# Performance work log

Measured on AMD Instinct MI355X. Metric: run time of the kernel, lower is better.

The kernel has to match this reference:

```python
import jax, jax.numpy as jnp
import numpy as np

N, E1, E2, P, H = 4096, 131072, 131072, 65536, 128
ROLE_VOCAB, ROLE_DIM, IDX_VOCAB, IDX_DIM = 8, 16, 1024, 8


def _lin_init(key, fan_in, fan_out):
    k1, k2 = jax.random.split(key)
    bound = 1.0 / np.sqrt(fan_in)
    W = jax.random.uniform(k1, (fan_in, fan_out), jnp.float32, -bound, bound)
    b = jax.random.uniform(k2, (fan_out,), jnp.float32, -bound, bound)
    return W, b


def setup_inputs() -> dict:
    key = jax.random.key(0)
    ks = jax.random.split(key, 24)
    d = {}
    d["block_features"] = jax.random.normal(ks[0], (N, 16), jnp.float32)
    d["role_ids"] = jax.random.randint(ks[1], (N,), 0, ROLE_VOCAB)
    d["b2b_src"] = jax.random.randint(ks[2], (E1,), 0, N)
    d["b2b_dst"] = jax.random.randint(ks[3], (E1,), 0, N)
    d["b2b_w"] = jax.random.uniform(ks[4], (E1,), jnp.float32)
    d["p2b_pin"] = jax.random.randint(ks[5], (E2,), 0, P)
    d["p2b_block"] = jax.random.randint(ks[6], (E2,), 0, N)
    d["p2b_w"] = jax.random.uniform(ks[7], (E2,), jnp.float32)
    d["pins_pos"] = jax.random.normal(ks[8], (P, 2), jnp.float32)
    d["area_targets"] = jax.random.uniform(ks[9], (N,), jnp.float32)
    # parameters
    d["role_emb"] = jax.random.normal(ks[10], (ROLE_VOCAB, ROLE_DIM), jnp.float32)
    d["idx_emb"] = jax.random.normal(ks[11], (IDX_VOCAB, IDX_DIM), jnp.float32)
    d["in_W1"], d["in_b1"] = _lin_init(ks[12], 16 + IDX_DIM + ROLE_DIM, H)
    d["in_W2"], d["in_b2"] = _lin_init(ks[13], H, H)
    d["b2b_W1"], d["b2b_b1"] = _lin_init(ks[14], 2 * H + 1, H)
    d["b2b_W2"], d["b2b_b2"] = _lin_init(ks[15], H, H)
    d["p2b_W1"], d["p2b_b1"] = _lin_init(ks[16], H + 3, H)
    d["p2b_W2"], d["p2b_b2"] = _lin_init(ks[17], H, H)
    d["self_W"], d["self_b"] = _lin_init(ks[18], H, H)
    d["ln_g"] = jnp.ones((H,), jnp.float32)
    d["ln_b"] = jnp.zeros((H,), jnp.float32)
    d["gp_W1"], d["gp_b1"] = _lin_init(ks[19], 2 * H, H)
    d["gp_W2"], d["gp_b2"] = _lin_init(ks[20], H, H)
    return d


def _mlp2(x, W1, b1, W2, b2):
    return jax.nn.relu(x @ W1 + b1) @ W2 + b2


def _forward(block_features, role_ids, b2b_src, b2b_dst, b2b_w, p2b_pin, p2b_block,
             p2b_w, pins_pos, area_targets, role_emb, idx_emb, in_W1, in_b1, in_W2,
             in_b2, b2b_W1, b2b_b1, b2b_W2, b2b_b2, p2b_W1, p2b_b1, p2b_W2, p2b_b2,
             self_W, self_b, ln_g, ln_b, gp_W1, gp_b1, gp_W2, gp_b2):
    n = block_features.shape[0]
    role_e = role_emb[role_ids]                       # [N, role_dim]
    idx_e = idx_emb[jnp.arange(n) % IDX_VOCAB]        # [N, idx_dim]
    x = jnp.concatenate([block_features, role_e, idx_e], axis=-1)
    h = jax.nn.relu(_mlp2(x, in_W1, in_b1, in_W2, in_b2))  # input_proj ends in ReLU

    # --- b2b messages: two directed messages per undirected edge ---
    max_b2b = jax.lax.stop_gradient(jnp.maximum(jnp.max(jnp.abs(b2b_w)), 1.0))
    w = (b2b_w / max_b2b)[:, None]                    # [E1, 1]
    hi, hj = h[b2b_src], h[b2b_dst]                   # [E1, H]
    m_ij = _mlp2(jnp.concatenate([hi, hj, w], -1), b2b_W1, b2b_b1, b2b_W2, b2b_b2)
    m_ji = _mlp2(jnp.concatenate([hj, hi, w], -1), b2b_W1, b2b_b1, b2b_W2, b2b_b2)
    agg = jnp.zeros_like(h).at[b2b_src].add(m_ij).at[b2b_dst].add(m_ji)

    # --- p2b messages ---
    total_area = jnp.maximum(jnp.sum(area_targets), 1e-6)
    case_scale = jax.lax.stop_gradient(jnp.maximum(jnp.sqrt(total_area), 1e-6))
    max_p2b = jax.lax.stop_gradient(jnp.maximum(jnp.max(jnp.abs(p2b_w)), 1.0))
    pin_feats = jnp.concatenate(
        [pins_pos[p2b_pin] / case_scale, (p2b_w / max_p2b)[:, None]], axis=-1)  # [E2, 3]
    m_p = _mlp2(jnp.concatenate([h[p2b_block], pin_feats], -1),
                p2b_W1, p2b_b1, p2b_W2, p2b_b2)
    agg = agg.at[p2b_block].add(m_p)

    # --- combine + LayerNorm ---
    z = h @ self_W + self_b + agg
    mu = jnp.mean(z, axis=-1, keepdims=True)
    var = jnp.mean(jnp.square(z - mu), axis=-1, keepdims=True)
    block_embeddings = (z - mu) / jnp.sqrt(var + 1e-5) * ln_g + ln_b

    pooled = jnp.concatenate(
        [block_embeddings.mean(axis=0), block_embeddings.max(axis=0)], axis=-1)
    graph_embedding = _mlp2(pooled, gp_W1, gp_b1, gp_W2, gp_b2)
    return block_embeddings, graph_embedding


def reference(block_features, role_ids, b2b_src, b2b_dst, b2b_w, p2b_pin, p2b_block,
              p2b_w, pins_pos, area_targets, role_emb, idx_emb, in_W1, in_b1, in_W2,
              in_b2, b2b_W1, b2b_b1, b2b_W2, b2b_b2, p2b_W1, p2b_b1, p2b_W2, p2b_b2,
              self_W, self_b, ln_g, ln_b, gp_W1, gp_b1, gp_W2, gp_b2):
    block_embeddings, graph_embedding = _forward(
        block_features, role_ids, b2b_src, b2b_dst, b2b_w, p2b_pin, p2b_block,
        p2b_w, pins_pos, area_targets, role_emb, idx_emb, in_W1, in_b1, in_W2,
        in_b2, b2b_W1, b2b_b1, b2b_W2, b2b_b2, p2b_W1, p2b_b1, p2b_W2, p2b_b2,
        self_W, self_b, ln_g, ln_b, gp_W1, gp_b1, gp_W2, gp_b2)
    block_mask = jnp.ones((block_features.shape[0],), dtype=bool)
    return block_embeddings, graph_embedding, block_mask
```

## Files before the change

kernel.cpp:

```cpp
#include <hip/hip_runtime.h>
#include <hip/hip_bf16.h>

#define N_NODES 4096
#define HDIM    128
#define E1      131072
#define E2      131072
#define NMSG_B2B (2 * E1)
#define CAPB    192
#define CAPP    96
#define STGB    128
#define STGP    64

#define OFF_CNTB   8
#define OFF_CNTP   (OFF_CNTB + 4096)
#define OFF_RED    (OFF_CNTP + 4096)
#define OFF_PSUM   (OFF_RED + 96)
#define OFF_PMAX   (OFF_PSUM + 512)
#define OFF_HB     (OFF_PMAX + 512)
#define OFF_P      (OFF_HB + 262144)
#define OFF_Q      (OFF_P + 524288)
#define OFF_R      (OFF_Q + 524288)
#define OFF_CP     (OFF_R + 524288)
#define OFF_B2H    (OFF_CP + 24576)
#define OFF_B2L    (OFF_B2H + 8192)
#define OFF_P2H    (OFF_B2L + 8192)
#define OFF_P2L    (OFF_P2H + 8192)
#define OFF_SWP    (OFF_P2L + 8192)
#define OFF_IW1    (OFF_SWP + 8192)
#define OFF_IW2    (OFF_IW1 + 4096)
#define OFF_WLAST  (OFF_IW2 + 8192)
#define OFF_PEXTRA (OFF_WLAST + 128)
#define OFF_BKB    (OFF_PEXTRA + 384)
#define OFF_BKP    (OFF_BKB + 2 * N_NODES * CAPB)
#define WS_FLOATS  (OFF_BKP + 2 * N_NODES * CAPP)

typedef short short8 __attribute__((ext_vector_type(8)));
typedef float f32x4 __attribute__((ext_vector_type(4)));

__device__ __forceinline__ unsigned short f2bf(float f) {
  union { float f; unsigned u; } v; v.f = f;
  unsigned r = v.u + 0x7fffu + ((v.u >> 16) & 1u);
  return (unsigned short)(r >> 16);
}
__device__ __forceinline__ float bf2f(unsigned short h) {
  return __uint_as_float((unsigned)h << 16);
}
__device__ __forceinline__ int il(int c) { return ((c & 63) << 1) | (c >> 6); }
__device__ __forceinline__ f32x4 relu4(f32x4 v) {
  f32x4 r;
  r[0] = fmaxf(v[0], 0.f); r[1] = fmaxf(v[1], 0.f);
  r[2] = fmaxf(v[2], 0.f); r[3] = fmaxf(v[3], 0.f);
  return r;
}

__global__ __launch_bounds__(256) void setup_kernel(const float* __restrict__ b2bw,
                                                    const float* __restrict__ p2bw,
                                                    const float* __restrict__ area,
                                                    const float* __restrict__ bW1,
                                                    const float* __restrict__ bW2,
                                                    const float* __restrict__ pW1,
                                                    const float* __restrict__ pW2,
                                                    const float* __restrict__ sWm,
                                                    const float* __restrict__ iW1,
                                                    const float* __restrict__ iW2,
                                                    const int* __restrict__ src,
                                                    const int* __restrict__ dst,
                                                    const int* __restrict__ pblk,
                                                    const int* __restrict__ ppin,
                                                    const float* __restrict__ pins,
                                                    float* __restrict__ ws) {
  __shared__ float red[256];
  int b = blockIdx.x, t = threadIdx.x;
  if (b < 32) {
    float m = 0.f;
    for (int i = b * 256 + t; i < E1; i += 32 * 256) m = fmaxf(m, fabsf(b2bw[i]));
    red[t] = m; __syncthreads();
    for (int s = 128; s > 0; s >>= 1) { if (t < s) red[t] = fmaxf(red[t], red[t + s]); __syncthreads(); }
    if (t == 0) ws[OFF_RED + b] = red[0];
  } else if (b < 64) {
    float m = 0.f;
    for (int i = (b - 32) * 256 + t; i < E2; i += 32 * 256) m = fmaxf(m, fabsf(p2bw[i]));
    red[t] = m; __syncthreads();
    for (int s = 128; s > 0; s >>= 1) { if (t < s) red[t] = fmaxf(red[t], red[t + s]); __syncthreads(); }
    if (t == 0) ws[OFF_RED + b] = red[0];
  } else if (b < 96) {
    float s0 = 0.f;
    for (int i = (b - 64) * 256 + t; i < N_NODES; i += 32 * 256) s0 += area[i];
    red[t] = s0; __syncthreads();
    for (int s = 128; s > 0; s >>= 1) { if (t < s) red[t] += red[t + s]; __syncthreads(); }
    if (t == 0) ws[OFF_RED + b] = red[0];
  } else if (b == 96) {
    for (int i = t; i < 512; i += 256) {
      ws[OFF_PSUM + i] = 0.f;
      ((int*)ws)[OFF_PMAX + i] = 0x80000000;
    }
  } else if (b < 225) {
    unsigned short* Cp  = (unsigned short*)(ws + OFF_CP);
    unsigned short* B2h = (unsigned short*)(ws + OFF_B2H);
    unsigned short* B2l = (unsigned short*)(ws + OFF_B2L);
    unsigned short* P2h = (unsigned short*)(ws + OFF_P2H);
    unsigned short* P2l = (unsigned short*)(ws + OFF_P2L);
    unsigned short* Swp = (unsigned short*)(ws + OFF_SWP);
    unsigned short* I1p = (unsigned short*)(ws + OFF_IW1);
    unsigned short* I2p = (unsigned short*)(ws + OFF_IW2);
    float* wlast = ws + OFF_WLAST;
    float* pextra = ws + OFF_PEXTRA;
    const int total = 156160;
    for (int x = (b - 97) * 256 + t; x < total; x += 128 * 256) {
      if (x < 49152) {
        int j = x & 7, lane = (x >> 3) & 63, ks = (x >> 9) & 3, nc = x >> 11;
        int col = nc * 16 + (lane & 15), k = ks * 32 + (lane >> 4) * 8 + j;
        float v;
        if (col < 128)      v = bW1[k * 128 + col];
        else if (col < 256) v = bW1[(128 + k) * 128 + (col - 128)];
        else                v = pW1[k * 128 + (col - 256)];
        Cp[x] = f2bf(v);
      } else if (x < 114688) {
        int u = (x - 49152) & 16383, which = (x - 49152) >> 14;
        int j = u & 7, lane = (u >> 3) & 63, ks = (u >> 9) & 3, nt = u >> 11;
        int n = nt * 16 + (lane & 15), k = ks * 32 + (lane >> 4) * 8 + j;
        float v = (which < 2) ? bW2[k * 128 + n] : pW2[k * 128 + n];
        unsigned short hi = f2bf(v);
        unsigned short outv = (which & 1) ? f2bf(v - bf2f(hi)) : hi;
        ((which < 2) ? ((which & 1) ? B2l : B2h) : ((which & 1) ? P2l : P2h))[u] = outv;
      } else if (x < 131072) {
        int u = x - 114688;
        int j = u & 7, lane = (u >> 3) & 63, ks = (u >> 9) & 3, nt = u >> 11;
        int n = nt * 16 + (lane & 15), k = ks * 32 + (lane >> 4) * 8 + j;
        Swp[u] = f2bf(sWm[k * 128 + n]);
      } else if (x < 139264) {
        int u = x - 131072;
        int j = u & 7, lane = (u >> 3) & 63, ks = (u >> 9) & 1, nt = u >> 10;
        int n = nt * 16 + (lane & 15), k = ks * 32 + (lane >> 4) * 8 + j;
        I1p[u] = (k < 40) ? f2bf(iW1[k * 128 + n]) : 0;
      } else if (x < 155648) {
        int u = x - 139264;
        int j = u & 7, lane = (u >> 3) & 63, ks = (u >> 9) & 3, nt = u >> 11;
        int n = nt * 16 + (lane & 15), k = ks * 32 + (lane >> 4) * 8 + j;
        I2p[u] = f2bf(iW2[k * 128 + n]);
      } else if (x < 155776) {
        int c = x - 155648;
        wlast[il(c)] = bW1[256 * 128 + c];
      } else {
        int u = x - 155776;
        int r = u >> 7, c = u & 127;
        pextra[r * 128 + il(c)] = pW1[(128 + r) * 128 + c];
      }
    }
  } else {
    int i = (b - 225) * 256 + t;
    int* cntB = (int*)ws + OFF_CNTB;
    int* cntP = (int*)ws + OFF_CNTP;
    uint2* BKB = (uint2*)((int*)ws + OFF_BKB);
    uint2* BKP = (uint2*)((int*)ws + OFF_BKP);
    if (i < NMSG_B2B) {
      int e = i >> 1, d = i & 1;
      int tg = d ? dst[e] : src[e];
      int o  = d ? src[e] : dst[e];
      int pos = atomicAdd(&cntB[tg], 1);
      if (pos < CAPB) {
        uint2 v; v.x = (unsigned)o; v.y = __float_as_uint(b2bw[e]);
        BKB[tg * CAPB + pos] = v;
      }
    } else {
      int e = i - NMSG_B2B;
      int pin = ppin[e];
      int tg = pblk[e];
      int pos = atomicAdd(&cntP[tg], 1);
      if (pos < CAPP) {
        uint2 v;
        v.x = ((unsigned)f2bf(pins[pin * 2 + 1]) << 16) | (unsigned)f2bf(pins[pin * 2]);
        v.y = __float_as_uint(p2bw[e]);
        BKP[tg * CAPP + pos] = v;
      }
    }
  }
}

__global__ __launch_bounds__(512) void mid_kernel(const float* __restrict__ bfeat,
                                                  const int* __restrict__ rid,
                                                  const float* __restrict__ remb,
                                                  const float* __restrict__ iemb,
                                                  const float* __restrict__ ib1,
                                                  const float* __restrict__ ib2,
                                                  const float* __restrict__ bb1,
                                                  const float* __restrict__ pb1,
                                                  float* __restrict__ ws,
                                                  unsigned short* __restrict__ hb) {
  __shared__ __attribute__((aligned(16))) unsigned short xs[16 * 72];
  __shared__ __attribute__((aligned(16))) unsigned short h1s[16 * 136];
  __shared__ __attribute__((aligned(16))) unsigned short hs[16 * 136];
  int tid = threadIdx.x;
  const unsigned short* I1p = (const unsigned short*)(ws + OFF_IW1);
  const unsigned short* I2p = (const unsigned short*)(ws + OFF_IW2);
  const unsigned short* Cp  = (const unsigned short*)(ws + OFF_CP);
  float* P = ws + OFF_P;
  float* Q = ws + OFF_Q;
  float* R = ws + OFF_R;
  int n0 = blockIdx.x * 16;
  for (int idx = tid; idx < 1024; idx += 512) {
    int m = idx >> 6, c = idx & 63;
    int n = n0 + m;
    float v = 0.f;
    if (c < 16)      v = bfeat[n * 16 + c];
    else if (c < 32) v = remb[rid[n] * 16 + (c - 16)];
    else if (c < 40) v = iemb[(n & 1023) * 8 + (c - 32)];
    xs[m * 72 + c] = f2bf(v);
  }
  __syncthreads();
  int lane = tid & 63, wv = tid >> 6;
  int l15 = lane & 15, q = lane >> 4;
  f32x4 zero = {0.f, 0.f, 0.f, 0.f};
  f32x4 a1 = zero;
#pragma unroll
  for (int ks = 0; ks < 2; ks++) {
    short8 af = *(const short8*)(&xs[l15 * 72 + ks * 32 + q * 8]);
    short8 bfr = *(const short8*)(I1p + ((wv * 2 + ks) * 64 + lane) * 8);
    a1 = __builtin_amdgcn_mfma_f32_16x16x32_bf16(af, bfr, a1, 0, 0, 0);
  }
  {
    int n = wv * 16 + l15;
    float b = ib1[n];
#pragma unroll
    for (int r = 0; r < 4; r++)
      h1s[(q * 4 + r) * 136 + n] = f2bf(fmaxf(a1[r] + b, 0.f));
  }
  __syncthreads();
  f32x4 a2 = zero;
#pragma unroll
  for (int ks = 0; ks < 4; ks++) {
    short8 af = *(const short8*)(&h1s[l15 * 136 + ks * 32 + q * 8]);
    short8 bfr = *(const short8*)(I2p + ((wv * 4 + ks) * 64 + lane) * 8);
    a2 = __builtin_amdgcn_mfma_f32_16x16x32_bf16(af, bfr, a2, 0, 0, 0);
  }
  {
    int n = wv * 16 + l15;
    float b = ib2[n];
#pragma unroll
    for (int r = 0; r < 4; r++) {
      unsigned short hv = f2bf(fmaxf(a2[r] + b, 0.f));
      hs[(q * 4 + r) * 136 + n] = hv;
      hb[(n0 + q * 4 + r) * 128 + n] = hv;
    }
  }
  __syncthreads();
  f32x4 a3[3];
#pragma unroll
  for (int i = 0; i < 3; i++) a3[i] = zero;
#pragma unroll
  for (int ks = 0; ks < 4; ks++) {
    short8 af = *(const short8*)(&hs[l15 * 136 + ks * 32 + q * 8]);
#pragma unroll
    for (int j = 0; j < 3; j++) {
      short8 bfr = *(const short8*)(Cp + (((3 * wv + j) * 4 + ks) * 64 + lane) * 8);
      a3[j] = __builtin_amdgcn_mfma_f32_16x16x32_bf16(af, bfr, a3[j], 0, 0, 0);
    }
  }
#pragma unroll
  for (int j = 0; j < 3; j++) {
    int col = (3 * wv + j) * 16 + l15;
    int arr = col >> 7, cc = col & 127;
    float bias = (arr == 0) ? bb1[cc] : ((arr == 2) ? pb1[cc] : 0.f);
    float* dstp = (arr == 0) ? P : ((arr == 1) ? Q : R);
    int ic = il(cc);
#pragma unroll
    for (int r = 0; r < 4; r++)
      dstp[(n0 + q * 4 + r) * 128 + ic] = a3[j][r] + bias;
  }
}

__global__ __launch_bounds__(1024) void fused_kernel(const unsigned short* __restrict__ hb,
                                                     const float* __restrict__ sb,
                                                     const float* __restrict__ lng,
                                                     const float* __restrict__ lnb,
                                                     const float* __restrict__ bb2,
                                                     const float* __restrict__ pb2,
                                                     const float* __restrict__ gW1,
                                                     const float* __restrict__ gb1,
                                                     const float* __restrict__ gW2,
                                                     const float* __restrict__ gb2,
                                                     float* __restrict__ ws,
                                                     float* __restrict__ out) {
  __shared__ __attribute__((aligned(16))) unsigned short A[16 * 648];
  __shared__ __attribute__((aligned(16))) union {
    struct { float zp[2][16 * 128]; float zs[16 * 133]; } t;
    struct { uint2 bkb[16][STGB]; uint2 bkp[16][STGP]; } e;
  } U;
  __shared__ float muS[16], rsg[16];
  __shared__ float partS[16][16], partQ[16][16];
  __shared__ float psumL[8][128];
  __shared__ int   pmaxL[8][128];
  __shared__ float sInvB, sInvP, sInvC;
  __shared__ int   isLast;
  int tid = threadIdx.x;
  int n0 = blockIdx.x * 16;
  int lane = tid & 63, wv = tid >> 6;
  const int* cntBp = (const int*)ws + OFF_CNTB;
  const int* cntPp = (const int*)ws + OFF_CNTP;
  const uint2* BKB = (const uint2*)((const int*)ws + OFF_BKB);
  const uint2* BKP = (const uint2*)((const int*)ws + OFF_BKP);
  if (tid < 256) {
    int m = tid >> 4, o = (tid & 15) * 8;
    *(uint4*)(&A[m * 648 + o]) = *(const uint4*)(hb + (n0 + m) * 128 + o);
  }
  for (int idx = tid; idx < 16 * STGB; idx += 1024) {
    int m = idx >> 7, j = idx & (STGB - 1);
    if (j < cntBp[n0 + m]) U.e.bkb[m][j] = BKB[(n0 + m) * CAPB + j];
  }
  {
    int m = tid >> 6, j = tid & (STGP - 1);
    if (tid < 16 * STGP && j < cntPp[n0 + m]) U.e.bkp[m][j] = BKP[(n0 + m) * CAPP + j];
  }
  if (tid < 96) {
    float v = ws[OFF_RED + tid];
    if (tid < 64) {
#pragma unroll
      for (int s = 1; s < 32; s <<= 1) v = fmaxf(v, __shfl_xor(v, s, 64));
      if (tid == 0)  sInvB = 1.f / fmaxf(v, 1.f);
      if (tid == 32) sInvP = 1.f / fmaxf(v, 1.f);
    } else {
#pragma unroll
      for (int s = 1; s < 32; s <<= 1) v += __shfl_xor(v, s, 64);
      if (tid == 64) {
        float cs = fmaxf(sqrtf(fmaxf(v, 1e-6f)), 1e-6f);
        sInvC = 1.f / cs;
      }
    }
  }
  int l5 = lane & 31, hf = lane >> 5;
  f32x4 wl = *(const f32x4*)(ws + OFF_WLAST + 4 * l5);
  f32x4 e0 = *(const f32x4*)(ws + OFF_PEXTRA + 4 * l5);
  f32x4 e1 = *(const f32x4*)(ws + OFF_PEXTRA + 128 + 4 * l5);
  f32x4 e2 = *(const f32x4*)(ws + OFF_PEXTRA + 256 + 4 * l5);
  __syncthreads();
  {
    const float* Pm = ws + OFF_P;
    const float* Qm = ws + OFF_Q;
    const float* Rm = ws + OFF_R;
    float invb = sInvB, invp = sInvP, invc = sInvC;
    wl *= invb; e0 *= invc; e1 *= invc; e2 *= invp;
    int ln = wv;
    int node = n0 + ln;
    {
      int cnt = min(cntBp[node], CAPB);
      int stg = min(cnt, STGB);
      const uint2* bkL = U.e.bkb[ln];
      const uint2* bkG = BKB + node * CAPB;
      f32x4 p4 = *(const f32x4*)(Pm + node * 128 + 4 * l5);
      f32x4 acc = {0.f, 0.f, 0.f, 0.f};
      int m = 0;
      for (; m + 16 <= stg; m += 16) {
        uint2 k0 = bkL[m + hf],      k1 = bkL[m + 2 + hf];
        uint2 k2 = bkL[m + 4 + hf],  k3 = bkL[m + 6 + hf];
        uint2 k4 = bkL[m + 8 + hf],  k5 = bkL[m + 10 + hf];
        uint2 k6 = bkL[m + 12 + hf], k7 = bkL[m + 14 + hf];
        f32x4 q0 = *(const f32x4*)(Qm + k0.x * 128 + 4 * l5);
        f32x4 q1 = *(const f32x4*)(Qm + k1.x * 128 + 4 * l5);
        f32x4 q2 = *(const f32x4*)(Qm + k2.x * 128 + 4 * l5);
        f32x4 q3 = *(const f32x4*)(Qm + k3.x * 128 + 4 * l5);
        f32x4 q4 = *(const f32x4*)(Qm + k4.x * 128 + 4 * l5);
        f32x4 q5 = *(const f32x4*)(Qm + k5.x * 128 + 4 * l5);
        f32x4 q6 = *(const f32x4*)(Qm + k6.x * 128 + 4 * l5);
        f32x4 q7 = *(const f32x4*)(Qm + k7.x * 128 + 4 * l5);
        acc += relu4(p4 + __uint_as_float(k0.y) * wl + q0);
        acc += relu4(p4 + __uint_as_float(k1.y) * wl + q1);
        acc += relu4(p4 + __uint_as_float(k2.y) * wl + q2);
        acc += relu4(p4 + __uint_as_float(k3.y) * wl + q3);
        acc += relu4(p4 + __uint_as_float(k4.y) * wl + q4);
        acc += relu4(p4 + __uint_as_float(k5.y) * wl + q5);
        acc += relu4(p4 + __uint_as_float(k6.y) * wl + q6);
        acc += relu4(p4 + __uint_as_float(k7.y) * wl + q7);
      }
      for (; m + 8 <= stg; m += 8) {
        uint2 k0 = bkL[m + hf],     k1 = bkL[m + 2 + hf];
        uint2 k2 = bkL[m + 4 + hf], k3 = bkL[m + 6 + hf];
        f32x4 q0 = *(const f32x4*)(Qm + k0.x * 128 + 4 * l5);
        f32x4 q1 = *(const f32x4*)(Qm + k1.x * 128 + 4 * l5);
        f32x4 q2 = *(const f32x4*)(Qm + k2.x * 128 + 4 * l5);
        f32x4 q3 = *(const f32x4*)(Qm + k3.x * 128 + 4 * l5);
        acc += relu4(p4 + __uint_as_float(k0.y) * wl + q0);
        acc += relu4(p4 + __uint_as_float(k1.y) * wl + q1);
        acc += relu4(p4 + __uint_as_float(k2.y) * wl + q2);
        acc += relu4(p4 + __uint_as_float(k3.y) * wl + q3);
      }
      for (; m + 2 <= stg; m += 2) {
        uint2 k = bkL[m + hf];
        f32x4 q = *(const f32x4*)(Qm + k.x * 128 + 4 * l5);
        acc += relu4(p4 + __uint_as_float(k.y) * wl + q);
      }
      if (m < stg) {
        uint2 k = bkL[m + hf];
        f32x4 q = *(const f32x4*)(Qm + (k.x & (N_NODES - 1)) * 128 + 4 * l5);
        f32x4 v = relu4(p4 + __uint_as_float(k.y) * wl + q);
        if (hf == 0) acc += v;
        m++;
      }
      for (; m + 2 <= cnt; m += 2) {
        uint2 k = bkG[m + hf];
        f32x4 q = *(const f32x4*)(Qm + k.x * 128 + 4 * l5);
        acc += relu4(p4 + __uint_as_float(k.y) * wl + q);
      }
      if (m < cnt) {
        uint2 k = bkG[m + hf];
        f32x4 q = *(const f32x4*)(Qm + (k.x & (N_NODES - 1)) * 128 + 4 * l5);
        f32x4 v = relu4(p4 + __uint_as_float(k.y) * wl + q);
        if (hf == 0) acc += v;
      }
      f32x4 tot;
#pragma unroll
      for (int j = 0; j < 4; j++) tot[j] = acc[j] + __shfl_xor(acc[j], 32, 64);
      if (hf == 0) {
        unsigned short h0 = f2bf(tot[0]), h1 = f2bf(tot[1]);
        unsigned short h2 = f2bf(tot[2]), h3 = f2bf(tot[3]);
        *(unsigned*)(&A[ln * 648 + 128 + 2 * l5])      = (unsigned)h0 | ((unsigned)h2 << 16);
        *(unsigned*)(&A[ln * 648 + 128 + 64 + 2 * l5]) = (unsigned)h1 | ((unsigned)h3 << 16);
        unsigned short g0 = f2bf(tot[0] - bf2f(h0)), g1 = f2bf(tot[1] - bf2f(h1));
        unsigned short g2 = f2bf(tot[2] - bf2f(h2)), g3 = f2bf(tot[3] - bf2f(h3));
        *(unsigned*)(&A[ln * 648 + 256 + 2 * l5])      = (unsigned)g0 | ((unsigned)g2 << 16);
        *(unsigned*)(&A[ln * 648 + 256 + 64 + 2 * l5]) = (unsigned)g1 | ((unsigned)g3 << 16);
      }
    }
    {
      int cnt = min(cntPp[node], CAPP);
      int stg = min(cnt, STGP);
      const uint2* bkL = U.e.bkp[ln];
      const uint2* bkG = BKP + node * CAPP;
      f32x4 r4 = *(const f32x4*)(Rm + node * 128 + 4 * l5);
      f32x4 acc = {0.f, 0.f, 0.f, 0.f};
      int m = 0;
      for (; m + 4 <= stg; m += 4) {
        uint2 ka = bkL[m + hf], kb = bkL[m + 2 + hf];
        float a0 = __uint_as_float((ka.x & 0xFFFFu) << 16);
        float a1 = __uint_as_float(ka.x & 0xFFFF0000u);
        float a2 = __uint_as_float(ka.y);
        float b0 = __uint_as_float((kb.x & 0xFFFFu) << 16);
        float b1 = __uint_as_float(kb.x & 0xFFFF0000u);
        float b2 = __uint_as_float(kb.y);
        acc += relu4(r4 + a0 * e0 + a1 * e1 + a2 * e2);
        acc += relu4(r4 + b0 * e0 + b1 * e1 + b2 * e2);
      }
      for (; m + 2 <= stg; m += 2) {
        uint2 ka = bkL[m + hf];
        float a0 = __uint_as_float((ka.x & 0xFFFFu) << 16);
        float a1 = __uint_as_float(ka.x & 0xFFFF0000u);
        float a2 = __uint_as_float(ka.y);
        acc += relu4(r4 + a0 * e0 + a1 * e1 + a2 * e2);
      }
      if (m < stg) {
        uint2 ka = bkL[m + hf];
        float a0 = __uint_as_float((ka.x & 0xFFFFu) << 16);
        float a1 = __uint_as_float(ka.x & 0xFFFF0000u);
        float a2 = __uint_as_float(ka.y);
        f32x4 v = relu4(r4 + a0 * e0 + a1 * e1 + a2 * e2);
        if (hf == 0) acc += v;
        m++;
      }
      for (; m + 2 <= cnt; m += 2) {
        uint2 ka = bkG[m + hf];
        float a0 = __uint_as_float((ka.x & 0xFFFFu) << 16);
        float a1 = __uint_as_float(ka.x & 0xFFFF0000u);
        float a2 = __uint_as_float(ka.y);
        acc += relu4(r4 + a0 * e0 + a1 * e1 + a2 * e2);
      }
      if (m < cnt) {
        uint2 ka = bkG[m + hf];
        float a0 = __uint_as_float((ka.x & 0xFFFFu) << 16);
        float a1 = __uint_as_float(ka.x & 0xFFFF0000u);
        float a2 = __uint_as_float(ka.y);
        f32x4 v = relu4(r4 + a0 * e0 + a1 * e1 + a2 * e2);
        if (hf == 0) acc += v;
      }
      f32x4 tot;
#pragma unroll
      for (int j = 0; j < 4; j++) tot[j] = acc[j] + __shfl_xor(acc[j], 32, 64);
      if (hf == 0) {
        unsigned short h0 = f2bf(tot[0]), h1 = f2bf(tot[1]);
        unsigned short h2 = f2bf(tot[2]), h3 = f2bf(tot[3]);
        *(unsigned*)(&A[ln * 648 + 384 + 2 * l5])      = (unsigned)h0 | ((unsigned)h2 << 16);
        *(unsigned*)(&A[ln * 648 + 384 + 64 + 2 * l5]) = (unsigned)h1 | ((unsigned)h3 << 16);
        unsigned short g0 = f2bf(tot[0] - bf2f(h0)), g1 = f2bf(tot[1] - bf2f(h1));
        unsigned short g2 = f2bf(tot[2] - bf2f(h2)), g3 = f2bf(tot[3] - bf2f(h3));
        *(unsigned*)(&A[ln * 648 + 512 + 2 * l5])      = (unsigned)g0 | ((unsigned)g2 << 16);
        *(unsigned*)(&A[ln * 648 + 512 + 64 + 2 * l5]) = (unsigned)g1 | ((unsigned)g3 << 16);
      }
    }
  }
  __syncthreads();
  int l15 = lane & 15, q = lane >> 4;
  int ct = wv & 7, half = wv >> 3;
  f32x4 zero = {0.f, 0.f, 0.f, 0.f};
  f32x4 acc = zero;
  const unsigned short* bufs[7] = {
    (const unsigned short*)(ws + OFF_SWP), (const unsigned short*)(ws + OFF_B2H),
    (const unsigned short*)(ws + OFF_B2L), (const unsigned short*)(ws + OFF_B2H),
    (const unsigned short*)(ws + OFF_P2H), (const unsigned short*)(ws + OFF_P2L),
    (const unsigned short*)(ws + OFF_P2H)};
  const int segs[7] = {0, 128, 128, 256, 384, 384, 512};
  int p0 = half ? 4 : 0, p1 = half ? 7 : 4;
  for (int p = p0; p < p1; p++) {
#pragma unroll
    for (int ks = 0; ks < 4; ks++) {
      short8 af = *(const short8*)(&A[l15 * 648 + segs[p] + ks * 32 + q * 8]);
      short8 bfr = *(const short8*)(bufs[p] + ((ct * 4 + ks) * 64 + lane) * 8);
      acc = __builtin_amdgcn_mfma_f32_16x16x32_bf16(af, bfr, acc, 0, 0, 0);
    }
  }
  {
    int nn = ct * 16 + l15;
#pragma unroll
    for (int r = 0; r < 4; r++)
      U.t.zp[half][(q * 4 + r) * 128 + nn] = acc[r];
  }
  __syncthreads();
  {
    int idx = tid;
    for (int rep = 0; rep < 2; rep++, idx += 1024) {
      int row = idx >> 7, c = idx & 127;
      float cb = (float)cntBp[n0 + row], cp = (float)cntPp[n0 + row];
      U.t.zs[row * 133 + c] = U.t.zp[0][row * 128 + c] + U.t.zp[1][row * 128 + c]
                            + sb[c] + cb * bb2[c] + cp * pb2[c];
    }
  }
  __syncthreads();
  if (tid < 256) {
    int r = tid >> 4, g = tid & 15;
    const float* zr = &U.t.zs[r * 133 + g * 8];
    float s = 0.f, s2 = 0.f;
#pragma unroll
    for (int i = 0; i < 8; i++) { float v = zr[i]; s += v; s2 += v * v; }
    partS[r][g] = s; partQ[r][g] = s2;
  }
  __syncthreads();
  if (tid < 16) {
    float s = 0.f, s2 = 0.f;
#pragma unroll
    for (int g = 0; g < 16; g++) { s += partS[tid][g]; s2 += partQ[tid][g]; }
    float m = s * (1.f / 128.f);
    float var = s2 * (1.f / 128.f) - m * m;
    muS[tid] = m;
    rsg[tid] = rsqrtf(fmaxf(var, 0.f) + 1e-5f);
  }
  __syncthreads();
  {
    int c = tid & 127, grp = tid >> 7;
    float g = lng[c], b = lnb[c];
    float ls = 0.f; int lm = 0x80000000;
    for (int r = grp * 2; r < grp * 2 + 2; r++) {
      float v = (U.t.zs[r * 133 + c] - muS[r]) * rsg[r] * g + b;
      out[(n0 + r) * 128 + c] = v;
      ls += v;
      int e = __float_as_int(v);
      e = e >= 0 ? e : (e ^ 0x7fffffff);
      lm = max(lm, e);
    }
    psumL[grp][c] = ls; pmaxL[grp][c] = lm;
  }
  __syncthreads();
  if (tid < 128) {
    float s = 0.f; int mx = 0x80000000;
#pragma unroll
    for (int g = 0; g < 8; g++) { s += psumL[g][tid]; mx = max(mx, pmaxL[g][tid]); }
    int bank = (blockIdx.x & 3) << 7;
    atomicAdd(&ws[OFF_PSUM + bank + tid], s);
    atomicMax(&((int*)ws)[OFF_PMAX + bank + tid], mx);
  }
  if (tid < 16) out[N_NODES * HDIM + HDIM + n0 + tid] = 1.0f;
  __syncthreads();
  if (tid == 0) {
    __threadfence();
    int v = atomicAdd(&((int*)ws)[3], 1);
    isLast = (v == (int)gridDim.x - 1);
  }
  __syncthreads();
  if (!isLast) return;
  __shared__ float pooled[256];
  __shared__ float gpart[8][128];
  __shared__ float g1[128];
  if (tid < 128) {
    float s = 0.f;
#pragma unroll
    for (int bk = 0; bk < 4; bk++) s += atomicAdd(&ws[OFF_PSUM + bk * 128 + tid], 0.f);
    pooled[tid] = s * (1.f / (float)N_NODES);
  } else if (tid < 256) {
    int c = tid - 128;
    int mx = 0x80000000;
#pragma unroll
    for (int bk = 0; bk < 4; bk++) mx = max(mx, atomicAdd(&((int*)ws)[OFF_PMAX + bk * 128 + c], 0));
    int bits = mx >= 0 ? mx : (mx ^ 0x7fffffff);
    pooled[tid] = __int_as_float(bits);
  }
  __syncthreads();
  {
    int c = tid & 127, g = tid >> 7;
    float acc2 = 0.f;
#pragma unroll 8
    for (int k = g * 32; k < g * 32 + 32; k++) acc2 += pooled[k] * gW1[k * 128 + c];
    gpart[g][c] = acc2;
  }
  __syncthreads();
  if (tid < 128) {
    float s = gb1[tid];
#pragma unroll
    for (int g = 0; g < 8; g++) s += gpart[g][tid];
    g1[tid] = fmaxf(s, 0.f);
  }
  __syncthreads();
  {
    int c = tid & 127, g = tid >> 7;
    float acc2 = 0.f;
#pragma unroll 8
    for (int k = g * 16; k < g * 16 + 16; k++) acc2 += g1[k] * gW2[k * 128 + c];
    gpart[g][c] = acc2;
  }
  __syncthreads();
  if (tid < 128) {
    float s = gb2[tid];
#pragma unroll
    for (int g = 0; g < 8; g++) s += gpart[g][tid];
    out[N_NODES * HDIM + tid] = s;
  }
}

extern "C" void kernel_launch(void* const* d_in, const int* in_sizes, int n_in,
                              void* d_out, int out_size, void* d_ws, size_t ws_size,
                              hipStream_t stream) {
  const float* bfeat = (const float*)d_in[0];
  const int*   rid   = (const int*)d_in[1];
  const int*   bsrc  = (const int*)d_in[2];
  const int*   bdst  = (const int*)d_in[3];
  const float* bw    = (const float*)d_in[4];
  const int*   ppin  = (const int*)d_in[5];
  const int*   pblk  = (const int*)d_in[6];
  const float* pw    = (const float*)d_in[7];
  const float* pins  = (const float*)d_in[8];
  const float* area  = (const float*)d_in[9];
  const float* remb  = (const float*)d_in[10];
  const float* iemb  = (const float*)d_in[11];
  const float* inW1  = (const float*)d_in[12];
  const float* inb1  = (const float*)d_in[13];
  const float* inW2  = (const float*)d_in[14];
  const float* inb2  = (const float*)d_in[15];
  const float* bW1   = (const float*)d_in[16];
  const float* bb1   = (const float*)d_in[17];
  const float* bW2   = (const float*)d_in[18];
  const float* bb2   = (const float*)d_in[19];
  const float* pW1   = (const float*)d_in[20];
  const float* pb1   = (const float*)d_in[21];
  const float* pW2   = (const float*)d_in[22];
  const float* pb2   = (const float*)d_in[23];
  const float* sW    = (const float*)d_in[24];
  const float* sb    = (const float*)d_in[25];
  const float* lng   = (const float*)d_in[26];
  const float* lnb   = (const float*)d_in[27];
  const float* gW1   = (const float*)d_in[28];
  const float* gb1   = (const float*)d_in[29];
  const float* gW2   = (const float*)d_in[30];
  const float* gb2   = (const float*)d_in[31];

  float* ws  = (float*)d_ws;
  float* out = (float*)d_out;
  unsigned short* hb = (unsigned short*)(ws + OFF_HB);

  hipMemsetAsync(d_ws, 0, OFF_RED * sizeof(float), stream);
  setup_kernel<<<1761, 256, 0, stream>>>(bw, pw, area,
                                         bW1, bW2, pW1, pW2, sW, inW1, inW2,
                                         bsrc, bdst, pblk, ppin, pins, ws);
  mid_kernel<<<256, 512, 0, stream>>>(bfeat, rid, remb, iemb, inb1, inb2, bb1, pb1,
                                      ws, hb);
  fused_kernel<<<256, 1024, 0, stream>>>(hb, sb, lng, lnb, bb2, pb2,
                                         gW1, gb1, gW2, gb2, ws, out);
}
```

Before: 183.6 us.

## Merge input MLP kernel into fused kernel via cooperative grid sync

```diff
diff --git a/kernel.cpp b/kernel.cpp
--- a/kernel.cpp
+++ b/kernel.cpp
@@ -1,5 +1,6 @@
 #include <hip/hip_runtime.h>
 #include <hip/hip_bf16.h>
+#include <hip/hip_cooperative_groups.h>
 
 #define N_NODES 4096
 #define HDIM    128
@@ -177,114 +178,36 @@
   }
 }
 
-__global__ __launch_bounds__(512) void mid_kernel(const float* __restrict__ bfeat,
-                                                  const int* __restrict__ rid,
-                                                  const float* __restrict__ remb,
-                                                  const float* __restrict__ iemb,
-                                                  const float* __restrict__ ib1,
-                                                  const float* __restrict__ ib2,
-                                                  const float* __restrict__ bb1,
-                                                  const float* __restrict__ pb1,
-                                                  float* __restrict__ ws,
-                                                  unsigned short* __restrict__ hb) {
-  __shared__ __attribute__((aligned(16))) unsigned short xs[16 * 72];
-  __shared__ __attribute__((aligned(16))) unsigned short h1s[16 * 136];
-  __shared__ __attribute__((aligned(16))) unsigned short hs[16 * 136];
-  int tid = threadIdx.x;
-  const unsigned short* I1p = (const unsigned short*)(ws + OFF_IW1);
-  const unsigned short* I2p = (const unsigned short*)(ws + OFF_IW2);
-  const unsigned short* Cp  = (const unsigned short*)(ws + OFF_CP);
-  float* P = ws + OFF_P;
-  float* Q = ws + OFF_Q;
-  float* R = ws + OFF_R;
-  int n0 = blockIdx.x * 16;
-  for (int idx = tid; idx < 1024; idx += 512) {
-    int m = idx >> 6, c = idx & 63;
-    int n = n0 + m;
-    float v = 0.f;
-    if (c < 16)      v = bfeat[n * 16 + c];
-    else if (c < 32) v = remb[rid[n] * 16 + (c - 16)];
-    else if (c < 40) v = iemb[(n & 1023) * 8 + (c - 32)];
-    xs[m * 72 + c] = f2bf(v);
-  }
-  __syncthreads();
-  int lane = tid & 63, wv = tid >> 6;
-  int l15 = lane & 15, q = lane >> 4;
-  f32x4 zero = {0.f, 0.f, 0.f, 0.f};
-  f32x4 a1 = zero;
-#pragma unroll
-  for (int ks = 0; ks < 2; ks++) {
-    short8 af = *(const short8*)(&xs[l15 * 72 + ks * 32 + q * 8]);
-    short8 bfr = *(const short8*)(I1p + ((wv * 2 + ks) * 64 + lane) * 8);
-    a1 = __builtin_amdgcn_mfma_f32_16x16x32_bf16(af, bfr, a1, 0, 0, 0);
-  }
-  {
-    int n = wv * 16 + l15;
-    float b = ib1[n];
-#pragma unroll
-    for (int r = 0; r < 4; r++)
-      h1s[(q * 4 + r) * 136 + n] = f2bf(fmaxf(a1[r] + b, 0.f));
-  }
-  __syncthreads();
-  f32x4 a2 = zero;
-#pragma unroll
-  for (int ks = 0; ks < 4; ks++) {
-    short8 af = *(const short8*)(&h1s[l15 * 136 + ks * 32 + q * 8]);
-    short8 bfr = *(const short8*)(I2p + ((wv * 4 + ks) * 64 + lane) * 8);
-    a2 = __builtin_amdgcn_mfma_f32_16x16x32_bf16(af, bfr, a2, 0, 0, 0);
-  }
-  {
-    int n = wv * 16 + l15;
-    float b = ib2[n];
-#pragma unroll
-    for (int r = 0; r < 4; r++) {
-      unsigned short hv = f2bf(fmaxf(a2[r] + b, 0.f));
-      hs[(q * 4 + r) * 136 + n] = hv;
-      hb[(n0 + q * 4 + r) * 128 + n] = hv;
-    }
-  }
-  __syncthreads();
-  f32x4 a3[3];
-#pragma unroll
-  for (int i = 0; i < 3; i++) a3[i] = zero;
-#pragma unroll
-  for (int ks = 0; ks < 4; ks++) {
-    short8 af = *(const short8*)(&hs[l15 * 136 + ks * 32 + q * 8]);
-#pragma unroll
-    for (int j = 0; j < 3; j++) {
-      short8 bfr = *(const short8*)(Cp + (((3 * wv + j) * 4 + ks) * 64 + lane) * 8);
-      a3[j] = __builtin_amdgcn_mfma_f32_16x16x32_bf16(af, bfr, a3[j], 0, 0, 0);
-    }
-  }
-#pragma unroll
-  for (int j = 0; j < 3; j++) {
-    int col = (3 * wv + j) * 16 + l15;
-    int arr = col >> 7, cc = col & 127;
-    float bias = (arr == 0) ? bb1[cc] : ((arr == 2) ? pb1[cc] : 0.f);
-    float* dstp = (arr == 0) ? P : ((arr == 1) ? Q : R);
-    int ic = il(cc);
-#pragma unroll
-    for (int r = 0; r < 4; r++)
-      dstp[(n0 + q * 4 + r) * 128 + ic] = a3[j][r] + bias;
-  }
-}
-
-__global__ __launch_bounds__(1024) void fused_kernel(const unsigned short* __restrict__ hb,
-                                                     const float* __restrict__ sb,
-                                                     const float* __restrict__ lng,
-                                                     const float* __restrict__ lnb,
-                                                     const float* __restrict__ bb2,
-                                                     const float* __restrict__ pb2,
-                                                     const float* __restrict__ gW1,
-                                                     const float* __restrict__ gb1,
-                                                     const float* __restrict__ gW2,
-                                                     const float* __restrict__ gb2,
-                                                     float* __restrict__ ws,
-                                                     float* __restrict__ out) {
+__global__ __launch_bounds__(1024) void mlpfused_kernel(const float* __restrict__ bfeat,
+                                                        const int* __restrict__ rid,
+                                                        const float* __restrict__ remb,
+                                                        const float* __restrict__ iemb,
+                                                        const float* __restrict__ ib1,
+                                                        const float* __restrict__ ib2,
+                                                        const float* __restrict__ bb1,
+                                                        const float* __restrict__ pb1,
+                                                        const float* __restrict__ sb,
+                                                        const float* __restrict__ lng,
+                                                        const float* __restrict__ lnb,
+                                                        const float* __restrict__ bb2,
+                                                        const float* __restrict__ pb2,
+                                                        const float* __restrict__ gW1,
+                                                        const float* __restrict__ gb1,
+                                                        const float* __restrict__ gW2,
+                                                        const float* __restrict__ gb2,
+                                                        float* __restrict__ ws,
+                                                        float* __restrict__ out) {
   __shared__ __attribute__((aligned(16))) unsigned short A[16 * 648];
   __shared__ __attribute__((aligned(16))) union {
+    struct {
+      uint2 bkb[16][STGB];
+      uint2 bkp[16][STGP];
+      float Pl[16][128];
+      float Rl[16][128];
+      unsigned short xs[16 * 72];
+      unsigned short h1s[16 * 136];
+    } e;
     struct { float zp[2][16 * 128]; float zs[16 * 133]; } t;
-    struct { uint2 bkb[16][STGB]; uint2 bkp[16][STGP]; } e;
   } U;
   __shared__ float muS[16], rsg[16];
   __shared__ float partS[16][16], partQ[16][16];
@@ -299,46 +222,121 @@
   const int* cntPp = (const int*)ws + OFF_CNTP;
   const uint2* BKB = (const uint2*)((const int*)ws + OFF_BKB);
   const uint2* BKP = (const uint2*)((const int*)ws + OFF_BKP);
-  if (tid < 256) {
-    int m = tid >> 4, o = (tid & 15) * 8;
-    *(uint4*)(&A[m * 648 + o]) = *(const uint4*)(hb + (n0 + m) * 128 + o);
-  }
-  for (int idx = tid; idx < 16 * STGB; idx += 1024) {
-    int m = idx >> 7, j = idx & (STGB - 1);
-    if (j < cntBp[n0 + m]) U.e.bkb[m][j] = BKB[(n0 + m) * CAPB + j];
-  }
+  const unsigned short* I1p = (const unsigned short*)(ws + OFF_IW1);
+  const unsigned short* I2p = (const unsigned short*)(ws + OFF_IW2);
+  const unsigned short* Cp  = (const unsigned short*)(ws + OFF_CP);
+  float* Qm = ws + OFF_Q;
+  int l15 = lane & 15, q = lane >> 4;
+  f32x4 zero = {0.f, 0.f, 0.f, 0.f};
+  if (wv < 8) {
+    for (int idx = tid; idx < 1024; idx += 512) {
+      int m = idx >> 6, c = idx & 63;
+      int n = n0 + m;
+      float v = 0.f;
+      if (c < 16)      v = bfeat[n * 16 + c];
+      else if (c < 32) v = remb[rid[n] * 16 + (c - 16)];
+      else if (c < 40) v = iemb[(n & 1023) * 8 + (c - 32)];
+      U.e.xs[m * 72 + c] = f2bf(v);
+    }
+  } else {
+    int u = tid - 512;
+    for (int idx = u; idx < 16 * STGB; idx += 512) {
+      int m = idx >> 7, j = idx & (STGB - 1);
+      if (j < cntBp[n0 + m]) U.e.bkb[m][j] = BKB[(n0 + m) * CAPB + j];
+    }
+  }
+  __syncthreads();
+  if (wv < 8) {
+    f32x4 a1 = zero;
+#pragma unroll
+    for (int ks = 0; ks < 2; ks++) {
+      short8 af = *(const short8*)(&U.e.xs[l15 * 72 + ks * 32 + q * 8]);
+      short8 bfr = *(const short8*)(I1p + ((wv * 2 + ks) * 64 + lane) * 8);
+      a1 = __builtin_amdgcn_mfma_f32_16x16x32_bf16(af, bfr, a1, 0, 0, 0);
+    }
+    int nW = wv * 16 + l15;
+    float bv = ib1[nW];
+#pragma unroll
+    for (int r = 0; r < 4; r++)
+      U.e.h1s[(q * 4 + r) * 136 + nW] = f2bf(fmaxf(a1[r] + bv, 0.f));
+  } else {
+    int u = tid - 512;
+    for (int idx = u; idx < 16 * STGP; idx += 512) {
+      int m = idx >> 6, j = idx & (STGP - 1);
+      if (j < cntPp[n0 + m]) U.e.bkp[m][j] = BKP[(n0 + m) * CAPP + j];
+    }
+    if (u < 96) {
+      float v = ws[OFF_RED + u];
+      if (u < 64) {
+#pragma unroll
+        for (int s = 1; s < 32; s <<= 1) v = fmaxf(v, __shfl_xor(v, s, 64));
+        if (u == 0)  sInvB = 1.f / fmaxf(v, 1.f);
+        if (u == 32) sInvP = 1.f / fmaxf(v, 1.f);
+      } else {
+#pragma unroll
+        for (int s = 1; s < 32; s <<= 1) v += __shfl_xor(v, s, 64);
+        if (u == 64) {
+          float cs = fmaxf(sqrtf(fmaxf(v, 1e-6f)), 1e-6f);
+          sInvC = 1.f / cs;
+        }
+      }
+    }
+  }
+  __syncthreads();
+  if (wv < 8) {
+    f32x4 a2 = zero;
+#pragma unroll
+    for (int ks = 0; ks < 4; ks++) {
+      short8 af = *(const short8*)(&U.e.h1s[l15 * 136 + ks * 32 + q * 8]);
+      short8 bfr = *(const short8*)(I2p + ((wv * 4 + ks) * 64 + lane) * 8);
+      a2 = __builtin_amdgcn_mfma_f32_16x16x32_bf16(af, bfr, a2, 0, 0, 0);
+    }
+    int nW = wv * 16 + l15;
+    float bv = ib2[nW];
+#pragma unroll
+    for (int r = 0; r < 4; r++)
+      A[(q * 4 + r) * 648 + nW] = f2bf(fmaxf(a2[r] + bv, 0.f));
+  }
+  __syncthreads();
+  if (wv < 8) {
+    f32x4 a3[3];
+#pragma unroll
+    for (int i = 0; i < 3; i++) a3[i] = zero;
+#pragma unroll
+    for (int ks = 0; ks < 4; ks++) {
+      short8 af = *(const short8*)(&A[l15 * 648 + ks * 32 + q * 8]);
+#pragma unroll
+      for (int j = 0; j < 3; j++) {
+        short8 bfr = *(const short8*)(Cp + (((3 * wv + j) * 4 + ks) * 64 + lane) * 8);
+        a3[j] = __builtin_amdgcn_mfma_f32_16x16x32_bf16(af, bfr, a3[j], 0, 0, 0);
+      }
+    }
+#pragma unroll
+    for (int j = 0; j < 3; j++) {
+      int col = (3 * wv + j) * 16 + l15;
+      int arr = col >> 7, cc = col & 127;
+      float bias = (arr == 0) ? bb1[cc] : ((arr == 2) ? pb1[cc] : 0.f);
+      int ic = il(cc);
+#pragma unroll
+      for (int r = 0; r < 4; r++) {
+        float val = a3[j][r] + bias;
+        int row = q * 4 + r;
+        if (arr == 0)      U.e.Pl[row][ic] = val;
+        else if (arr == 2) U.e.Rl[row][ic] = val;
+        else               Qm[(n0 + row) * 128 + ic] = val;
+      }
+    }
+  }
+  __threadfence();
+  cooperative_groups::this_grid().sync();
+  __threadfence();
+  int l5 = lane & 31, hf = lane >> 5;
   {
-    int m = tid >> 6, j = tid & (STGP - 1);
-    if (tid < 16 * STGP && j < cntPp[n0 + m]) U.e.bkp[m][j] = BKP[(n0 + m) * CAPP + j];
-  }
-  if (tid < 96) {
-    float v = ws[OFF_RED + tid];
-    if (tid < 64) {
-#pragma unroll
-      for (int s = 1; s < 32; s <<= 1) v = fmaxf(v, __shfl_xor(v, s, 64));
-      if (tid == 0)  sInvB = 1.f / fmaxf(v, 1.f);
-      if (tid == 32) sInvP = 1.f / fmaxf(v, 1.f);
-    } else {
-#pragma unroll
-      for (int s = 1; s < 32; s <<= 1) v += __shfl_xor(v, s, 64);
-      if (tid == 64) {
-        float cs = fmaxf(sqrtf(fmaxf(v, 1e-6f)), 1e-6f);
-        sInvC = 1.f / cs;
-      }
-    }
-  }
-  int l5 = lane & 31, hf = lane >> 5;
-  f32x4 wl = *(const f32x4*)(ws + OFF_WLAST + 4 * l5);
-  f32x4 e0 = *(const f32x4*)(ws + OFF_PEXTRA + 4 * l5);
-  f32x4 e1 = *(const f32x4*)(ws + OFF_PEXTRA + 128 + 4 * l5);
-  f32x4 e2 = *(const f32x4*)(ws + OFF_PEXTRA + 256 + 4 * l5);
-  __syncthreads();
-  {
-    const float* Pm = ws + OFF_P;
-    const float* Qm = ws + OFF_Q;
-    const float* Rm = ws + OFF_R;
-    float invb = sInvB, invp = sInvP, invc = sInvC;
-    wl *= invb; e0 *= invc; e1 *= invc; e2 *= invp;
+    f32x4 wl = *(const f32x4*)(ws + OFF_WLAST + 4 * l5);
+    f32x4 e0 = *(const f32x4*)(ws + OFF_PEXTRA + 4 * l5);
+    f32x4 e1 = *(const f32x4*)(ws + OFF_PEXTRA + 128 + 4 * l5);
+    f32x4 e2 = *(const f32x4*)(ws + OFF_PEXTRA + 256 + 4 * l5);
+    wl *= sInvB; e0 *= sInvC; e1 *= sInvC; e2 *= sInvP;
     int ln = wv;
     int node = n0 + ln;
     {
@@ -346,7 +344,7 @@
       int stg = min(cnt, STGB);
       const uint2* bkL = U.e.bkb[ln];
       const uint2* bkG = BKB + node * CAPB;
-      f32x4 p4 = *(const f32x4*)(Pm + node * 128 + 4 * l5);
+      f32x4 p4 = *(const f32x4*)(&U.e.Pl[ln][4 * l5]);
       f32x4 acc = {0.f, 0.f, 0.f, 0.f};
       int m = 0;
       for (; m + 16 <= stg; m += 16) {
@@ -385,25 +383,25 @@
       }
       for (; m + 2 <= stg; m += 2) {
         uint2 k = bkL[m + hf];
-        f32x4 q = *(const f32x4*)(Qm + k.x * 128 + 4 * l5);
-        acc += relu4(p4 + __uint_as_float(k.y) * wl + q);
+        f32x4 qv = *(const f32x4*)(Qm + k.x * 128 + 4 * l5);
+        acc += relu4(p4 + __uint_as_float(k.y) * wl + qv);
       }
       if (m < stg) {
         uint2 k = bkL[m + hf];
-        f32x4 q = *(const f32x4*)(Qm + (k.x & (N_NODES - 1)) * 128 + 4 * l5);
-        f32x4 v = relu4(p4 + __uint_as_float(k.y) * wl + q);
+        f32x4 qv = *(const f32x4*)(Qm + (k.x & (N_NODES - 1)) * 128 + 4 * l5);
+        f32x4 v = relu4(p4 + __uint_as_float(k.y) * wl + qv);
         if (hf == 0) acc += v;
         m++;
       }
       for (; m + 2 <= cnt; m += 2) {
         uint2 k = bkG[m + hf];
-        f32x4 q = *(const f32x4*)(Qm + k.x * 128 + 4 * l5);
-        acc += relu4(p4 + __uint_as_float(k.y) * wl + q);
+        f32x4 qv = *(const f32x4*)(Qm + k.x * 128 + 4 * l5);
+        acc += relu4(p4 + __uint_as_float(k.y) * wl + qv);
       }
       if (m < cnt) {
         uint2 k = bkG[m + hf];
-        f32x4 q = *(const f32x4*)(Qm + (k.x & (N_NODES - 1)) * 128 + 4 * l5);
-        f32x4 v = relu4(p4 + __uint_as_float(k.y) * wl + q);
+        f32x4 qv = *(const f32x4*)(Qm + (k.x & (N_NODES - 1)) * 128 + 4 * l5);
+        f32x4 v = relu4(p4 + __uint_as_float(k.y) * wl + qv);
         if (hf == 0) acc += v;
       }
       f32x4 tot;
@@ -425,7 +423,7 @@
       int stg = min(cnt, STGP);
       const uint2* bkL = U.e.bkp[ln];
       const uint2* bkG = BKP + node * CAPP;
-      f32x4 r4 = *(const f32x4*)(Rm + node * 128 + 4 * l5);
+      f32x4 r4 = *(const f32x4*)(&U.e.Rl[ln][4 * l5]);
       f32x4 acc = {0.f, 0.f, 0.f, 0.f};
       int m = 0;
       for (; m + 4 <= stg; m += 4) {
@@ -486,9 +484,7 @@
     }
   }
   __syncthreads();
-  int l15 = lane & 15, q = lane >> 4;
   int ct = wv & 7, half = wv >> 3;
-  f32x4 zero = {0.f, 0.f, 0.f, 0.f};
   f32x4 acc = zero;
   const unsigned short* bufs[7] = {
     (const unsigned short*)(ws + OFF_SWP), (const unsigned short*)(ws + OFF_B2H),
@@ -659,14 +655,17 @@
 
   float* ws  = (float*)d_ws;
   float* out = (float*)d_out;
-  unsigned short* hb = (unsigned short*)(ws + OFF_HB);
 
   hipMemsetAsync(d_ws, 0, OFF_RED * sizeof(float), stream);
   setup_kernel<<<1761, 256, 0, stream>>>(bw, pw, area,
                                          bW1, bW2, pW1, pW2, sW, inW1, inW2,
                                          bsrc, bdst, pblk, ppin, pins, ws);
-  mid_kernel<<<256, 512, 0, stream>>>(bfeat, rid, remb, iemb, inb1, inb2, bb1, pb1,
-                                      ws, hb);
-  fused_kernel<<<256, 1024, 0, stream>>>(hb, sb, lng, lnb, bb2, pb2,
-                                         gW1, gb1, gW2, gb2, ws, out);
+  void* args[] = {
+    (void*)&bfeat, (void*)&rid, (void*)&remb, (void*)&iemb,
+    (void*)&inb1, (void*)&inb2, (void*)&bb1, (void*)&pb1,
+    (void*)&sb, (void*)&lng, (void*)&lnb, (void*)&bb2, (void*)&pb2,
+    (void*)&gW1, (void*)&gb1, (void*)&gW2, (void*)&gb2,
+    (void*)&ws, (void*)&out};
+  hipLaunchCooperativeKernel((const void*)mlpfused_kernel, dim3(256), dim3(1024),
+                             args, 0, stream);
 }
```

After: 411.2 us. 2.24x slower.
